# Performance work log

Measured on AMD Instinct MI355X. Metric: run time of the kernel, lower is better.

## Reference

```python
import jax, jax.numpy as jnp
import numpy as np

B, N, DX, DZ, L = 512, 32, 78, 64, 1000

def _gcn_norm(A):
    # PyG gcn_norm: add remaining self loops (fill 1), symmetric D^-1/2 (A+I) D^-1/2
    n = A.shape[-1]
    A_hat = jnp.maximum(A, jnp.eye(n, dtype=A.dtype))
    dinv = jax.lax.rsqrt(A_hat.sum(-1))
    return A_hat * dinv[..., :, None] * dinv[..., None, :]

def _bn(h, g, b, eps=1e-5):
    # BatchNorm1d, training-mode batch statistics (torch default module state)
    m = jnp.mean(h, 0)
    v = jnp.var(h, 0)
    return (h - m) * jax.lax.rsqrt(v + eps) * g + b

def _conv(h, W, b):  # h [B,C,L], W [O,I,K], valid padding + ReLU (Conv1dReLU)
    y = jax.lax.conv_general_dilated(h, W, (1,), 'VALID', dimension_numbers=('NCH', 'OIH', 'NCH'))
    return jax.nn.relu(y + b[None, :, None])

def _attn(v):  # Attention.project is only Tanh in the source
    return jax.nn.softmax(jnp.tanh(v), axis=1) * v

def _forward(x, adj, target, z, dec_W0, dec_b0, dec_g0, dec_be0, dec_W1, dec_b1, dec_g1, dec_be1,
             gW1, gb1, gW2, gb2, gW3, gb3, fcg1_W, fcg1_b, fcg2_W, fcg2_b, emb,
             c10_W, c10_b, c20_W, c20_b, c21_W, c21_b, c30_W, c30_b, c31_W, c31_b, c32_W, c32_b,
             prot_W, prot_b, fc1_W, fc1_b, fc2_W, fc2_b, out_W, out_b):
    Bn = B * N
    # frozen conditional VAE decoder -> augmented features (detached)
    zc = jnp.concatenate([z.reshape(Bn, DZ), x.reshape(Bn, DX)], axis=-1)
    h = jax.nn.relu(_bn(zc @ dec_W0 + dec_b0, dec_g0, dec_be0))
    aug = jnp.tanh(_bn(h @ dec_W1 + dec_b1, dec_g1, dec_be1))
    aug = jax.lax.stop_gradient(aug).reshape(B, N, DX)
    X = jnp.concatenate([aug, x], axis=-1)  # [B,N,156]
    # 1-hop / 2-hop / 3-hop adjacency patterns (spspmm -> binary power patterns)
    A1 = _gcn_norm(adj)
    A2p = (adj @ adj > 0).astype(adj.dtype)
    A3p = (A2p @ adj > 0).astype(adj.dtype)
    A2 = _gcn_norm(A2p)
    A3 = _gcn_norm(A3p)
    gcn = lambda A, hh, W, b: jax.nn.relu(A @ (hh @ W) + b)
    h1 = gcn(A1, X, gW1, gb1)
    h2 = gcn(A1, h1, gW2, gb2)
    h3 = gcn(A1, h2, gW3, gb3)
    h5 = gcn(A2, gcn(A2, X, gW1, gb1), gW2, gb2)
    h6 = gcn(A3, X, gW1, gb1)
    hg = jnp.max(jnp.concatenate([h3, h5, h6], axis=-1), axis=1)  # gmp -> [B,1092]
    xg = jax.nn.relu(hg @ fcg1_W + fcg1_b) @ fcg2_W + fcg2_b  # dropout = identity (eval)
    xg = _attn(xg)
    # protein branch
    e = jnp.transpose(emb[target], (0, 2, 1))  # [B,128,1000]
    f1 = jnp.max(_conv(e, c10_W, c10_b), axis=-1)
    f2 = jnp.max(_conv(_conv(e, c20_W, c20_b), c21_W, c21_b), axis=-1)
    f3 = jnp.max(_conv(_conv(_conv(e, c30_W, c30_b), c31_W, c31_b), c32_W, c32_b), axis=-1)
    xt = _attn(jnp.concatenate([f1, f2, f3], axis=-1) @ prot_W + prot_b)
    xc = jnp.concatenate([xg, xt], axis=-1)
    xc = jax.nn.relu(xc @ fc1_W + fc1_b)
    xc = jax.nn.relu(xc @ fc2_W + fc2_b)
    return xc @ out_W + out_b

def setup_inputs():
    key = jax.random.key(0)
    ks = iter(jax.random.split(key, 64))
    def w(shape, s=0.05):
        return jax.random.normal(next(ks), shape, dtype=jnp.float32) * s
    x = jax.random.normal(next(ks), (B, N, DX), dtype=jnp.float32)
    r = jax.random.uniform(next(ks), (B, N, N))
    up = jnp.triu((r < 0.08).astype(jnp.float32), 1)
    adj = up + jnp.swapaxes(up, 1, 2)  # symmetric, no self loops, avg degree ~5
    target = jax.random.randint(next(ks), (B, L), 0, 26, dtype=jnp.int32)
    z = jax.random.normal(next(ks), (B, N, DZ), dtype=jnp.float32)
    emb = w((26, 128), 1.0).at[0].set(0.0)  # padding_idx=0
    return dict(x=x, adj=adj, target=target, z=z,
        dec_W0=w((DZ + DX, 256)), dec_b0=jnp.zeros(256), dec_g0=jnp.ones(256), dec_be0=jnp.zeros(256),
        dec_W1=w((256, DX)), dec_b1=jnp.zeros(DX), dec_g1=jnp.ones(DX), dec_be1=jnp.zeros(DX),
        gW1=w((156, 156)), gb1=jnp.zeros(156), gW2=w((156, 312)), gb2=jnp.zeros(312),
        gW3=w((312, 624)), gb3=jnp.zeros(624),
        fcg1_W=w((1092, 1024)), fcg1_b=jnp.zeros(1024), fcg2_W=w((1024, 128)), fcg2_b=jnp.zeros(128),
        emb=emb,
        c10_W=w((96, 128, 3)), c10_b=jnp.zeros(96),
        c20_W=w((96, 128, 3)), c20_b=jnp.zeros(96), c21_W=w((96, 96, 3)), c21_b=jnp.zeros(96),
        c30_W=w((96, 128, 3)), c30_b=jnp.zeros(96), c31_W=w((96, 96, 3)), c31_b=jnp.zeros(96),
        c32_W=w((96, 96, 3)), c32_b=jnp.zeros(96),
        prot_W=w((288, 128)), prot_b=jnp.zeros(128),
        fc1_W=w((256, 1024)), fc1_b=jnp.zeros(1024), fc2_W=w((1024, 512)), fc2_b=jnp.zeros(512),
        out_W=w((512, 1)), out_b=jnp.zeros(1))

def reference(x, adj, target, z, dec_W0, dec_b0, dec_g0, dec_be0, dec_W1, dec_b1, dec_g1, dec_be1,
              gW1, gb1, gW2, gb2, gW3, gb3, fcg1_W, fcg1_b, fcg2_W, fcg2_b, emb,
              c10_W, c10_b, c20_W, c20_b, c21_W, c21_b, c30_W, c30_b, c31_W, c31_b, c32_W, c32_b,
              prot_W, prot_b, fc1_W, fc1_b, fc2_W, fc2_b, out_W, out_b):
    return _forward(x, adj, target, z, dec_W0, dec_b0, dec_g0, dec_be0, dec_W1, dec_b1, dec_g1, dec_be1,
                    gW1, gb1, gW2, gb2, gW3, gb3, fcg1_W, fcg1_b, fcg2_W, fcg2_b, emb,
                    c10_W, c10_b, c20_W, c20_b, c21_W, c21_b, c30_W, c30_b, c31_W, c31_b, c32_W, c32_b,
                    prot_W, prot_b, fc1_W, fc1_b, fc2_W, fc2_b, out_W, out_b)
```

## Files before the change

### kernel.cpp

```cpp
#include <hip/hip_runtime.h>

static constexpr size_t O_H0    = 0;
static constexpr size_t O_H1P   = 4194304;
static constexpr size_t O_X     = 5473216;
static constexpr size_t O_A1    = 8029120;
static constexpr size_t O_A2    = 8553408;
static constexpr size_t O_A3    = 9077696;
static constexpr size_t O_H4    = 9601984;
static constexpr size_t O_H6    = 12157888;
static constexpr size_t O_H1W2  = 14713792;
static constexpr size_t O_H2    = 19825600;
static constexpr size_t O_H2W3  = 24937408;
static constexpr size_t O_H3    = 35161024;
static constexpr size_t O_HG    = 45384640;
static constexpr size_t O_FCG1O = 45943744;
static constexpr size_t O_M     = 46468032;
static constexpr size_t O_F     = 46535424;
static constexpr size_t O_V     = 46682880;
static constexpr size_t O_XC    = 46748416;
static constexpr size_t O_FC1O  = 46879488;
static constexpr size_t O_FC2O  = 47403776;
static constexpr size_t O_PART  = 47665920;
static constexpr size_t O_MV    = 47698688;
static constexpr size_t O_BT21  = 47699712;
static constexpr size_t O_BT31  = 47727360;
static constexpr size_t O_W32T  = 47755008;
static constexpr size_t O_XW1  = O_H0;
static constexpr size_t O_SK   = O_H0;
static constexpr size_t O_H1   = O_X;
static constexpr size_t O_H4W2 = O_H1W2;
static constexpr size_t O_H5   = O_H2W3;
static constexpr size_t O_R10  = O_H1W2;
static constexpr size_t O_R20  = O_H1W2 + 1687296;
static constexpr size_t O_R30  = O_H1W2 + 3374592;
static constexpr size_t O_N21  = O_H2W3;
static constexpr size_t O_N31  = O_H2W3 + 5061888;

template<int AMODE, int ACT>
__global__ __launch_bounds__(256) void gemm_k(
    const float* __restrict__ A, const float* __restrict__ Bm,
    const float* __restrict__ bias, float* __restrict__ C,
    int M, int N, int K, const float* __restrict__ A2)
{
  __shared__ __align__(16) float sA[16 * 68];
  __shared__ __align__(16) float sB[16 * 68];
  const int tid = threadIdx.x;
  const int m0 = blockIdx.y * 64, n0 = blockIdx.x * 64;
  const int tx = tid & 15, ty = tid >> 4;
  float acc[4][4] = {};
  for (int k0 = 0; k0 < K; k0 += 16) {
#pragma unroll
    for (int s2 = 0; s2 < 4; s2++) {
      int idx = tid + s2 * 256;
      int am = idx >> 4, ak = idx & 15;
      int gm = m0 + am, gk = k0 + ak;
      float va = 0.f;
      if (gm < M && gk < K) {
        if (AMODE == 0) va = A[(size_t)gm * K + gk];
        else            va = (gk < 64) ? A[gm * 64 + gk] : A2[gm * 78 + gk - 64];
      }
      sA[ak * 68 + am] = va;
      int bk2 = idx >> 6, bn = idx & 63;
      int gk2 = k0 + bk2, gn = n0 + bn;
      float vb = 0.f;
      if (gk2 < K && gn < N) vb = Bm[(size_t)gk2 * N + gn];
      sB[bk2 * 68 + bn] = vb;
    }
    __syncthreads();
#pragma unroll
    for (int kk = 0; kk < 16; kk++) {
      const float4 a4 = *(const float4*)&sA[kk * 68 + ty * 4];
      const float4 b4 = *(const float4*)&sB[kk * 68 + tx * 4];
      const float ra[4] = {a4.x, a4.y, a4.z, a4.w};
      const float rb[4] = {b4.x, b4.y, b4.z, b4.w};
#pragma unroll
      for (int i2 = 0; i2 < 4; i2++)
#pragma unroll
        for (int j2 = 0; j2 < 4; j2++)
          acc[i2][j2] = fmaf(ra[i2], rb[j2], acc[i2][j2]);
    }
    __syncthreads();
  }
#pragma unroll
  for (int i2 = 0; i2 < 4; i2++) {
    int gm = m0 + ty * 4 + i2;
    if (gm >= M) continue;
#pragma unroll
    for (int j2 = 0; j2 < 4; j2++) {
      int gn = n0 + tx * 4 + j2;
      if (gn >= N) continue;
      float v = acc[i2][j2];
      if (bias) v += bias[gn];
      if (ACT == 1) v = fmaxf(v, 0.f);
      C[(size_t)gm * N + gn] = v;
    }
  }
}

__global__ __launch_bounds__(256) void gemm_sk(
    const float* __restrict__ A, const float* __restrict__ Bm,
    float* __restrict__ PT, int M, int N, int K, int KS)
{
  __shared__ __align__(16) float sA[16 * 68];
  __shared__ __align__(16) float sB[16 * 68];
  const int tid = threadIdx.x;
  const int m0 = blockIdx.y * 64, n0 = blockIdx.x * 64;
  const int kb = blockIdx.z * KS;
  const int ke = min(K, kb + KS);
  const int tx = tid & 15, ty = tid >> 4;
  float acc[4][4] = {};
  for (int k0 = kb; k0 < ke; k0 += 16) {
#pragma unroll
    for (int s2 = 0; s2 < 4; s2++) {
      int idx = tid + s2 * 256;
      int am = idx >> 4, ak = idx & 15;
      int gm = m0 + am, gk = k0 + ak;
      float va = 0.f;
      if (gm < M && gk < ke) va = A[(size_t)gm * K + gk];
      sA[ak * 68 + am] = va;
      int bk2 = idx >> 6, bn = idx & 63;
      int gk2 = k0 + bk2, gn = n0 + bn;
      float vb = 0.f;
      if (gk2 < ke && gn < N) vb = Bm[(size_t)gk2 * N + gn];
      sB[bk2 * 68 + bn] = vb;
    }
    __syncthreads();
#pragma unroll
    for (int kk = 0; kk < 16; kk++) {
      const float4 a4 = *(const float4*)&sA[kk * 68 + ty * 4];
      const float4 b4 = *(const float4*)&sB[kk * 68 + tx * 4];
      const float ra[4] = {a4.x, a4.y, a4.z, a4.w};
      const float rb[4] = {b4.x, b4.y, b4.z, b4.w};
#pragma unroll
      for (int i2 = 0; i2 < 4; i2++)
#pragma unroll
        for (int j2 = 0; j2 < 4; j2++)
          acc[i2][j2] = fmaf(ra[i2], rb[j2], acc[i2][j2]);
    }
    __syncthreads();
  }
  float* P = PT + (size_t)blockIdx.z * M * N;
#pragma unroll
  for (int i2 = 0; i2 < 4; i2++) {
    int gm = m0 + ty * 4 + i2;
    if (gm >= M) continue;
#pragma unroll
    for (int j2 = 0; j2 < 4; j2++) {
      int gn = n0 + tx * 4 + j2;
      if (gn >= N) continue;
      P[(size_t)gm * N + gn] = acc[i2][j2];
    }
  }
}

__global__ void skred_kernel(const float* __restrict__ PT, const float* __restrict__ bias,
                             float* __restrict__ C, int MN, int nmask, int S, int act)
{
  int i = blockIdx.x * 256 + threadIdx.x;
  if (i >= MN) return;
  float s = 0.f;
  for (int z = 0; z < S; z++) s += PT[(size_t)z * MN + i];
  if (bias) s += bias[i & nmask];
  if (act) s = fmaxf(s, 0.f);
  C[i] = s;
}

template<int AMODE, int ACT>
__global__ __launch_bounds__(256) void gemm2_k(
    const float* __restrict__ A, const float* __restrict__ Bm,
    const float* __restrict__ bias, float* __restrict__ C,
    int M, int N, int K, const float* __restrict__ A2)
{
  __shared__ __align__(16) float sA[16 * 132];
  __shared__ __align__(16) float sB[16 * 68];
  const int tid = threadIdx.x;
  const int m0 = blockIdx.y * 128, n0 = blockIdx.x * 64;
  const int tx = tid & 15, ty = tid >> 4;
  float acc[8][4] = {};
  for (int k0 = 0; k0 < K; k0 += 16) {
#pragma unroll
    for (int s2 = 0; s2 < 2; s2++) {
      int idx = tid + s2 * 256;
      int am = idx >> 2, kq = idx & 3;
      int gm = m0 + am;
#pragma unroll
      for (int j = 0; j < 4; j++) {
        int gk = k0 + kq * 4 + j;
        float va = 0.f;
        if (gm < M && gk < K) {
          if (AMODE == 0) va = A[(size_t)gm * K + gk];
          else            va = (gk < 64) ? A[gm * 64 + gk] : A2[gm * 78 + gk - 64];
        }
        sA[(kq * 4 + j) * 132 + am] = va;
      }
    }
    {
      int bk = tid >> 4, bn4 = tid & 15;
      int gk2 = k0 + bk;
#pragma unroll
      for (int j = 0; j < 4; j++) {
        int gn = n0 + bn4 * 4 + j;
        float vb = 0.f;
        if (gk2 < K && gn < N) vb = Bm[(size_t)gk2 * N + gn];
        sB[bk * 68 + bn4 * 4 + j] = vb;
      }
    }
    __syncthreads();
#pragma unroll
    for (int kk = 0; kk < 16; kk++) {
      const float4 a0 = *(const float4*)&sA[kk * 132 + ty * 8];
      const float4 a1 = *(const float4*)&sA[kk * 132 + ty * 8 + 4];
      const float4 b4 = *(const float4*)&sB[kk * 68 + tx * 4];
      const float ra[8] = {a0.x, a0.y, a0.z, a0.w, a1.x, a1.y, a1.z, a1.w};
      const float rb[4] = {b4.x, b4.y, b4.z, b4.w};
#pragma unroll
      for (int i2 = 0; i2 < 8; i2++)
#pragma unroll
        for (int j2 = 0; j2 < 4; j2++)
          acc[i2][j2] = fmaf(ra[i2], rb[j2], acc[i2][j2]);
    }
    __syncthreads();
  }
#pragma unroll
  for (int i2 = 0; i2 < 8; i2++) {
    int gm = m0 + ty * 8 + i2;
    if (gm >= M) continue;
#pragma unroll
    for (int j2 = 0; j2 < 4; j2++) {
      int gn = n0 + tx * 4 + j2;
      if (gn >= N) continue;
      float v = acc[i2][j2];
      if (bias) v += bias[gn];
      if (ACT == 1) v = fmaxf(v, 0.f);
      C[(size_t)gm * N + gn] = v;
    }
  }
}

template<int AMODE, int ACT>
__global__ __launch_bounds__(256) void gemm3_k(
    const float* __restrict__ A, const float* __restrict__ Bm,
    const float* __restrict__ bias, float* __restrict__ C,
    int M, int N, int K, const float* __restrict__ A2)
{
  __shared__ __align__(16) float sA[16][132];
  __shared__ __align__(16) float sB[16][132];
  const int tid = threadIdx.x;
  const int m0 = blockIdx.y * 128, n0 = blockIdx.x * 128;
  const int tx = tid & 15, ty = tid >> 4;
  float acc[8][8] = {};
  for (int k0 = 0; k0 < K; k0 += 16) {
    {
      int am = tid >> 1;
      int kq = (tid & 1) * 8;
      int gm = m0 + am;
#pragma unroll
      for (int j = 0; j < 8; j++) {
        int gk = k0 + kq + j;
        float va = 0.f;
        if (gm < M && gk < K) {
          if (AMODE == 0) va = A[(size_t)gm * K + gk];
          else            va = (gk < 64) ? A[gm * 64 + gk] : A2[gm * 78 + gk - 64];
        }
        sA[kq + j][am] = va;
      }
      int bk = tid >> 4;
      int bn = (tid & 15) * 8;
      int gk2 = k0 + bk;
#pragma unroll
      for (int j = 0; j < 8; j++) {
        int gn = n0 + bn + j;
        float vb = 0.f;
        if (gk2 < K && gn < N) vb = Bm[(size_t)gk2 * N + gn];
        sB[bk][bn + j] = vb;
      }
    }
    __syncthreads();
#pragma unroll
    for (int kk = 0; kk < 16; kk++) {
      const float4 a0 = *(const float4*)&sA[kk][ty * 4];
      const float4 a1 = *(const float4*)&sA[kk][64 + ty * 4];
      const float4 b0 = *(const float4*)&sB[kk][tx * 4];
      const float4 b1 = *(const float4*)&sB[kk][64 + tx * 4];
      const float ra[8] = {a0.x, a0.y, a0.z, a0.w, a1.x, a1.y, a1.z, a1.w};
      const float rb[8] = {b0.x, b0.y, b0.z, b0.w, b1.x, b1.y, b1.z, b1.w};
#pragma unroll
      for (int i = 0; i < 8; i++)
#pragma unroll
        for (int j = 0; j < 8; j++)
          acc[i][j] = fmaf(ra[i], rb[j], acc[i][j]);
    }
    __syncthreads();
  }
#pragma unroll
  for (int i = 0; i < 8; i++) {
    int gm = m0 + (i < 4 ? ty * 4 + i : 64 + ty * 4 + (i - 4));
    if (gm >= M) continue;
#pragma unroll
    for (int j = 0; j < 8; j++) {
      int gn = n0 + (j < 4 ? tx * 4 + j : 64 + tx * 4 + (j - 4));
      if (gn >= N) continue;
      float v = acc[i][j];
      if (bias) v += bias[gn];
      if (ACT == 1) v = fmaxf(v, 0.f);
      C[(size_t)gm * N + gn] = v;
    }
  }
}

__global__ __launch_bounds__(256) void bn_partial(const float* __restrict__ H,
    float* __restrict__ PS, float* __restrict__ PQ, int C)
{
  int c = blockIdx.x * 64 + (threadIdx.x & 63);
  int rg = threadIdx.x >> 6;
  __shared__ float sS[256], sQ[256];
  float s = 0.f, q = 0.f;
  if (c < C) {
    int base = blockIdx.y * 256 + rg;
    for (int t = 0; t < 64; t++) {
      float v = H[(size_t)(base + 4 * t) * C + c];
      s += v; q += v * v;
    }
  }
  sS[threadIdx.x] = s; sQ[threadIdx.x] = q;
  __syncthreads();
  if (threadIdx.x < 64 && c < C) {
    float ts = sS[threadIdx.x] + sS[threadIdx.x + 64] + sS[threadIdx.x + 128] + sS[threadIdx.x + 192];
    float tq = sQ[threadIdx.x] + sQ[threadIdx.x + 64] + sQ[threadIdx.x + 128] + sQ[threadIdx.x + 192];
    PS[blockIdx.y * C + c] = ts;
    PQ[blockIdx.y * C + c] = tq;
  }
}

__global__ void bn_final(const float* __restrict__ PS, const float* __restrict__ PQ,
                         float* __restrict__ MV, int C)
{
  int c = threadIdx.x;
  if (c >= C) return;
  float s = 0.f, q = 0.f;
  for (int y = 0; y < 64; y++) { s += PS[y * C + c]; q += PQ[y * C + c]; }
  float mean = s * (1.f / 16384.f);
  float var = q * (1.f / 16384.f) - mean * mean;
  MV[c] = mean; MV[256 + c] = var;
}

__global__ void bn_norm(const float* __restrict__ IN, float* __restrict__ OUT,
                        const float* __restrict__ MV, const float* __restrict__ g,
                        const float* __restrict__ bb, int C, int ostride, int total, int act)
{
  int idx = blockIdx.x * 256 + threadIdx.x;
  if (idx >= total) return;
  int r = idx / C, c = idx - r * C;
  float v = (IN[idx] - MV[c]) * (1.f / sqrtf(MV[256 + c] + 1e-5f)) * g[c] + bb[c];
  v = (act == 1) ? fmaxf(v, 0.f) : tanhf(v);
  OUT[(size_t)r * ostride + c] = v;
}

__global__ void xcopy_kernel(const float* __restrict__ x, float* __restrict__ X)
{
  int idx = blockIdx.x * 256 + threadIdx.x;
  if (idx >= 16384 * 78) return;
  int r = idx / 78, j = idx - r * 78;
  X[(size_t)r * 156 + 78 + j] = x[idx];
}

__global__ __launch_bounds__(1024) void adj_kernel(const float* __restrict__ adj,
    float* __restrict__ A1o, float* __restrict__ A2o, float* __restrict__ A3o)
{
  int b = blockIdx.x, t = threadIdx.x;
  int i = t >> 5, j = t & 31;
  __shared__ float sA[32][33], sP[32][33];
  __shared__ float sd1[32], sd2[32], sd3[32];
  float a = adj[b * 1024 + t];
  sA[i][j] = a;
  float ah = (i == j) ? fmaxf(a, 1.f) : a;
  float rs = ah;
#pragma unroll
  for (int m = 16; m >= 1; m >>= 1) rs += __shfl_xor(rs, m, 32);
  float di = 1.f / sqrtf(rs);
  if (j == 0) sd1[i] = di;
  __syncthreads();
  A1o[b * 1024 + t] = ah * di * sd1[j];
  float c2 = 0.f;
#pragma unroll
  for (int k = 0; k < 32; k++) c2 += sA[i][k] * sA[k][j];
  float p2 = (c2 > 0.f) ? 1.f : 0.f;
  sP[i][j] = p2;
  float ah2 = (i == j) ? 1.f : p2;
  float rs2 = ah2;
#pragma unroll
  for (int m = 16; m >= 1; m >>= 1) rs2 += __shfl_xor(rs2, m, 32);
  float di2 = 1.f / sqrtf(rs2);
  if (j == 0) sd2[i] = di2;
  __syncthreads();
  A2o[b * 1024 + t] = ah2 * di2 * sd2[j];
  float c3 = 0.f;
#pragma unroll
  for (int k = 0; k < 32; k++) c3 += sP[i][k] * sA[k][j];
  float p3 = (c3 > 0.f) ? 1.f : 0.f;
  float ah3 = (i == j) ? 1.f : p3;
  float rs3 = ah3;
#pragma unroll
  for (int m = 16; m >= 1; m >>= 1) rs3 += __shfl_xor(rs3, m, 32);
  float di3 = 1.f / sqrtf(rs3);
  if (j == 0) sd3[i] = di3;
  __syncthreads();
  A3o[b * 1024 + t] = ah3 * di3 * sd3[j];
}

__global__ __launch_bounds__(64) void agg_kernel(const float* __restrict__ A,
    const float* __restrict__ HW, const float* __restrict__ bias,
    float* __restrict__ OUT, int C)
{
  int b = blockIdx.y;
  int c = blockIdx.x * 64 + threadIdx.x;
  __shared__ float sAd[1024];
  for (int e = threadIdx.x; e < 1024; e += 64) sAd[e] = A[b * 1024 + e];
  __syncthreads();
  if (c >= C) return;
  float hw[32];
  const float* hp = HW + (size_t)b * 32 * C + c;
#pragma unroll
  for (int m = 0; m < 32; m++) hw[m] = hp[(size_t)m * C];
  float bv = bias[c];
#pragma unroll 2
  for (int n = 0; n < 32; n++) {
    float s = bv;
#pragma unroll
    for (int m = 0; m < 32; m++) s = fmaf(sAd[n * 32 + m], hw[m], s);
    OUT[(size_t)b * 32 * C + (size_t)n * C + c] = fmaxf(s, 0.f);
  }
}

__global__ void hg_kernel(const float* __restrict__ h3, const float* __restrict__ h5,
                          const float* __restrict__ h6, float* __restrict__ HG)
{
  int b = blockIdx.y;
  int c = blockIdx.x * 256 + threadIdx.x;
  if (c >= 1092) return;
  const float* p; int stride;
  if (c < 624)      { p = h3 + (size_t)b * 32 * 624 + c;          stride = 624; }
  else if (c < 936) { p = h5 + (size_t)b * 32 * 312 + (c - 624);  stride = 312; }
  else              { p = h6 + (size_t)b * 32 * 156 + (c - 936);  stride = 156; }
  float m = p[0];
#pragma unroll 4
  for (int n = 1; n < 32; n++) m = fmaxf(m, p[(size_t)n * stride]);
  HG[b * 1092 + c] = m;
}

__global__ __launch_bounds__(64) void attn_kernel(const float* __restrict__ V,
    float* __restrict__ OUT, int ostride, int ooff)
{
  int r = blockIdx.x, lane = threadIdx.x;
  float v0 = V[r * 128 + lane], v1 = V[r * 128 + 64 + lane];
  float e0 = expf(tanhf(v0)), e1 = expf(tanhf(v1));
  float s = e0 + e1;
#pragma unroll
  for (int m = 32; m >= 1; m >>= 1) s += __shfl_xor(s, m);
  float inv = 1.f / s;
  OUT[r * ostride + ooff + lane] = e0 * inv * v0;
  OUT[r * ostride + ooff + 64 + lane] = e1 * inv * v1;
}

__global__ void mtable_kernel(const float* __restrict__ emb, const float* __restrict__ W10,
    const float* __restrict__ W20, const float* __restrict__ W30, float* __restrict__ M)
{
  int idx = blockIdx.x * 256 + threadIdx.x;
  if (idx >= 3 * 3 * 26 * 96) return;
  int o = idx % 96, tok = (idx / 96) % 26, k = (idx / (96 * 26)) % 3, cv = idx / (96 * 26 * 3);
  const float* W = (cv == 0) ? W10 : ((cv == 1) ? W20 : W30);
  float s = 0.f;
#pragma unroll 4
  for (int i = 0; i < 128; i++) s = fmaf(emb[tok * 128 + i], W[(o * 128 + i) * 3 + k], s);
  M[idx] = s;
}

__global__ void rtable_kernel(const float* __restrict__ M,
    const float* __restrict__ b1, const float* __restrict__ b2, const float* __restrict__ b3,
    float* __restrict__ R1, float* __restrict__ R2, float* __restrict__ R3)
{
  int cv = blockIdx.y;
  int idx = blockIdx.x * 256 + threadIdx.x;
  if (idx >= 17576 * 96) return;
  int o = idx % 96, g = idx / 96;
  int t0 = g / 676, t1 = (g / 26) % 26, t2 = g % 26;
  const float* Mc = M + cv * 3 * 26 * 96;
  float v = ((cv == 0) ? b1 : ((cv == 1) ? b2 : b3))[o];
  v += Mc[(0 * 26 + t0) * 96 + o] + Mc[(1 * 26 + t1) * 96 + o] + Mc[(2 * 26 + t2) * 96 + o];
  float* R = (cv == 0) ? R1 : ((cv == 1) ? R2 : R3);
  R[idx] = fmaxf(v, 0.f);
}

__global__ void wtrans_kernel(const float* __restrict__ W, float* __restrict__ out, int mode)
{
  int e = blockIdx.x * 256 + threadIdx.x;
  if (e >= 96 * 96 * 3) return;
  int o, i, k;
  if (mode == 0) { i = e / 288; int r = e % 288; k = r / 96; o = r % 96; }
  else           { k = e / (96 * 96); i = (e / 96) % 96; o = e % 96; }
  out[e] = W[(o * 96 + i) * 3 + k];
}

__global__ __launch_bounds__(384) void conv3_fused(const int* __restrict__ target,
    const float* __restrict__ R10,
    const float* __restrict__ N21, const float* __restrict__ b21,
    const float* __restrict__ N31, const float* __restrict__ b31,
    const float* __restrict__ W32t, const float* __restrict__ b32, float* __restrict__ F)
{
  int b = blockIdx.y, tile = blockIdx.x;
  int l0 = tile * 64;
  int tid = threadIdx.x;
  __shared__ float sIn[96 * 67];
  __shared__ int sG[68];
  __shared__ float sR1[4 * 96], sR2[4 * 96];
  int ncols = min(66, 996 - l0);
  int n1    = min(66, 998 - l0);
  int nouts = min(64, 994 - l0);
  int ng    = min(68, 998 - l0);
  for (int p = tid; p < ng; p += 384) {
    int t0 = target[b * 1000 + l0 + p];
    int t1 = target[b * 1000 + l0 + p + 1];
    int t2 = target[b * 1000 + l0 + p + 2];
    sG[p] = (t0 * 26 + t1) * 26 + t2;
  }
  __syncthreads();
  {
    int i = tid % 96;
    int coff = tid / 96;
    float v1m = 0.f, v2m = 0.f;
    for (int c = coff; c < n1; c += 4) {
      v1m = fmaxf(v1m, R10[(size_t)sG[c] * 96 + i]);
      if (c < ncols) {
        int g0 = sG[c], g1 = sG[c + 1], g2 = sG[c + 2];
        float n3 = b31[i]
                 + N31[((size_t)g0 * 3 + 0) * 96 + i]
                 + N31[((size_t)g1 * 3 + 1) * 96 + i]
                 + N31[((size_t)g2 * 3 + 2) * 96 + i];
        sIn[i * 67 + c] = fmaxf(n3, 0.f);
        float n2 = b21[i]
                 + N21[((size_t)g0 * 3 + 0) * 96 + i]
                 + N21[((size_t)g1 * 3 + 1) * 96 + i]
                 + N21[((size_t)g2 * 3 + 2) * 96 + i];
        v2m = fmaxf(v2m, fmaxf(n2, 0.f));
      }
    }
    sR1[coff * 96 + i] = v1m;
    sR2[coff * 96 + i] = v2m;
  }
  __syncthreads();
  if (tid < 192) {
    int which = tid / 96, i = tid % 96;
    const float* r = which ? sR2 : sR1;
    float m = fmaxf(fmaxf(r[i], r[96 + i]), fmaxf(r[192 + i], r[288 + i]));
    atomicMax((unsigned int*)&F[b * 288 + which * 96 + i], __float_as_uint(m));
  }
  int wv = __builtin_amdgcn_readfirstlane(tid >> 6);
  int lane = tid & 63;
  int obase = wv * 16;
  float acc[16];
#pragma unroll
  for (int jj = 0; jj < 16; jj++) acc[jj] = b32[obase + jj];
#pragma unroll 1
  for (int k = 0; k < 3; k++) {
#pragma unroll 4
    for (int i = 0; i < 96; i++) {
      float xv = sIn[i * 67 + lane + k];
      const float* wp = W32t + ((size_t)(k * 96 + i)) * 96 + obase;
#pragma unroll
      for (int jj = 0; jj < 16; jj++) acc[jj] = fmaf(xv, wp[jj], acc[jj]);
    }
  }
  bool lok = lane < nouts;
#pragma unroll
  for (int jj = 0; jj < 16; jj++) {
    float v = lok ? fmaxf(acc[jj], 0.f) : 0.f;
#pragma unroll
    for (int m = 32; m >= 1; m >>= 1) v = fmaxf(v, __shfl_xor(v, m));
    if (lane == 0) atomicMax((unsigned int*)&F[b * 288 + 192 + obase + jj], __float_as_uint(v));
  }
}

__global__ __launch_bounds__(256) void outdot_kernel(const float* __restrict__ X,
    const float* __restrict__ W, const float* __restrict__ bptr, float* __restrict__ out)
{
  int r = blockIdx.x * 4 + (threadIdx.x >> 6);
  int lane = threadIdx.x & 63;
  float s = 0.f;
  for (int j = lane; j < 512; j += 64) s = fmaf(X[(size_t)r * 512 + j], W[j], s);
#pragma unroll
  for (int m = 32; m >= 1; m >>= 1) s += __shfl_xor(s, m);
  if (lane == 0) out[r] = s + bptr[0];
}

static inline void gemm(hipStream_t st, int AMODE, int ACT,
                        const float* A, const float* B, const float* bias, float* C,
                        int M, int N, int K, const float* A2 = nullptr)
{
  dim3 g((N + 63) / 64, (M + 63) / 64), blk(256);
  if (AMODE == 0 && ACT == 0)      gemm_k<0, 0><<<g, blk, 0, st>>>(A, B, bias, C, M, N, K, A2);
  else if (AMODE == 0 && ACT == 1) gemm_k<0, 1><<<g, blk, 0, st>>>(A, B, bias, C, M, N, K, A2);
  else                             gemm_k<1, 0><<<g, blk, 0, st>>>(A, B, bias, C, M, N, K, A2);
}

static inline void gemm2(hipStream_t st, int AMODE, int ACT,
                         const float* A, const float* B, const float* bias, float* C,
                         int M, int N, int K, const float* A2 = nullptr)
{
  dim3 g((N + 63) / 64, (M + 127) / 128), blk(256);
  if (AMODE == 0 && ACT == 0)      gemm2_k<0, 0><<<g, blk, 0, st>>>(A, B, bias, C, M, N, K, A2);
  else if (AMODE == 0 && ACT == 1) gemm2_k<0, 1><<<g, blk, 0, st>>>(A, B, bias, C, M, N, K, A2);
  else                             gemm2_k<1, 0><<<g, blk, 0, st>>>(A, B, bias, C, M, N, K, A2);
}

static inline void gemm3(hipStream_t st, int AMODE, int ACT,
                         const float* A, const float* B, const float* bias, float* C,
                         int M, int N, int K, const float* A2 = nullptr)
{
  dim3 g((N + 127) / 128, (M + 127) / 128), blk(256);
  if (AMODE == 0 && ACT == 0)      gemm3_k<0, 0><<<g, blk, 0, st>>>(A, B, bias, C, M, N, K, A2);
  else if (AMODE == 0 && ACT == 1) gemm3_k<0, 1><<<g, blk, 0, st>>>(A, B, bias, C, M, N, K, A2);
  else                             gemm3_k<1, 0><<<g, blk, 0, st>>>(A, B, bias, C, M, N, K, A2);
}

static inline void gemm_splitk(hipStream_t st, const float* A, const float* B,
                               const float* bias, float* C, int M, int N, int K,
                               int S, int act, float* PT)
{
  int KS = (K + S - 1) / S;
  dim3 g((N + 63) / 64, (M + 63) / 64, S);
  gemm_sk<<<g, 256, 0, st>>>(A, B, PT, M, N, K, KS);
  int MN = M * N;
  skred_kernel<<<(MN + 255) / 256, 256, 0, st>>>(PT, bias, C, MN, N - 1, S, act);
}

extern "C" void kernel_launch(void* const* d_in, const int* in_sizes, int n_in,
                              void* d_out, int out_size, void* d_ws, size_t ws_size,
                              hipStream_t stream)
{
  (void)in_sizes; (void)n_in; (void)out_size; (void)ws_size;
  const float* x      = (const float*)d_in[0];
  const float* adj    = (const float*)d_in[1];
  const int*   target = (const int*)  d_in[2];
  const float* z      = (const float*)d_in[3];
  const float* dec_W0 = (const float*)d_in[4];
  const float* dec_b0 = (const float*)d_in[5];
  const float* dec_g0 = (const float*)d_in[6];
  const float* dec_be0= (const float*)d_in[7];
  const float* dec_W1 = (const float*)d_in[8];
  const float* dec_b1 = (const float*)d_in[9];
  const float* dec_g1 = (const float*)d_in[10];
  const float* dec_be1= (const float*)d_in[11];
  const float* gW1    = (const float*)d_in[12];
  const float* gb1    = (const float*)d_in[13];
  const float* gW2    = (const float*)d_in[14];
  const float* gb2    = (const float*)d_in[15];
  const float* gW3    = (const float*)d_in[16];
  const float* gb3    = (const float*)d_in[17];
  const float* fcg1_W = (const float*)d_in[18];
  const float* fcg1_b = (const float*)d_in[19];
  const float* fcg2_W = (const float*)d_in[20];
  const float* fcg2_b = (const float*)d_in[21];
  const float* emb    = (const float*)d_in[22];
  const float* c10_W  = (const float*)d_in[23];
  const float* c10_b  = (const float*)d_in[24];
  const float* c20_W  = (const float*)d_in[25];
  const float* c20_b  = (const float*)d_in[26];
  const float* c21_W  = (const float*)d_in[27];
  const float* c21_b  = (const float*)d_in[28];
  const float* c30_W  = (const float*)d_in[29];
  const float* c30_b  = (const float*)d_in[30];
  const float* c31_W  = (const float*)d_in[31];
  const float* c31_b  = (const float*)d_in[32];
  const float* c32_W  = (const float*)d_in[33];
  const float* c32_b  = (const float*)d_in[34];
  const float* prot_W = (const float*)d_in[35];
  const float* prot_b = (const float*)d_in[36];
  const float* fc1_W  = (const float*)d_in[37];
  const float* fc1_b  = (const float*)d_in[38];
  const float* fc2_W  = (const float*)d_in[39];
  const float* fc2_b  = (const float*)d_in[40];
  const float* out_W  = (const float*)d_in[41];
  const float* out_b  = (const float*)d_in[42];
  float* out = (float*)d_out;
  float* ws = (float*)d_ws;

  float* H0   = ws + O_H0;   float* H1P  = ws + O_H1P;  float* X    = ws + O_X;
  float* A1   = ws + O_A1;   float* A2   = ws + O_A2;   float* A3   = ws + O_A3;
  float* XW1  = ws + O_XW1;  float* H1   = ws + O_H1;   float* H4   = ws + O_H4;
  float* H6   = ws + O_H6;   float* H1W2 = ws + O_H1W2; float* H2   = ws + O_H2;
  float* H2W3 = ws + O_H2W3; float* H3   = ws + O_H3;   float* H4W2 = ws + O_H4W2;
  float* H5   = ws + O_H5;   float* HG   = ws + O_HG;   float* FCG1O= ws + O_FCG1O;
  float* Mt   = ws + O_M;    float* F    = ws + O_F;    float* V    = ws + O_V;
  float* XC   = ws + O_XC;   float* FC1O = ws + O_FC1O; float* FC2O = ws + O_FC2O;
  float* PS   = ws + O_PART; float* PQ   = ws + O_PART + 16384;
  float* MV   = ws + O_MV;   float* SK   = ws + O_SK;
  float* R10  = ws + O_R10;  float* R20  = ws + O_R20;  float* R30  = ws + O_R30;
  float* N21  = ws + O_N21;  float* N31  = ws + O_N31;
  float* BT21 = ws + O_BT21; float* BT31 = ws + O_BT31; float* W32T = ws + O_W32T;

  gemm3(stream, 1, 0, z, dec_W0, dec_b0, H0, 16384, 256, 142, x);
  bn_partial<<<dim3(4, 64), 256, 0, stream>>>(H0, PS, PQ, 256);
  bn_final<<<1, 256, 0, stream>>>(PS, PQ, MV, 256);
  bn_norm<<<16384, 256, 0, stream>>>(H0, H0, MV, dec_g0, dec_be0, 256, 256, 16384 * 256, 1);
  gemm2(stream, 0, 0, H0, dec_W1, dec_b1, H1P, 16384, 78, 256);
  bn_partial<<<dim3(2, 64), 256, 0, stream>>>(H1P, PS, PQ, 78);
  bn_final<<<1, 256, 0, stream>>>(PS, PQ, MV, 78);
  bn_norm<<<4995, 256, 0, stream>>>(H1P, X, MV, dec_g1, dec_be1, 78, 156, 16384 * 78, 2);
  xcopy_kernel<<<4995, 256, 0, stream>>>(x, X);

  adj_kernel<<<512, 1024, 0, stream>>>(adj, A1, A2, A3);

  gemm2(stream, 0, 0, X, gW1, nullptr, XW1, 16384, 156, 156);
  agg_kernel<<<dim3(3, 512), 64, 0, stream>>>(A1, XW1, gb1, H1, 156);
  agg_kernel<<<dim3(3, 512), 64, 0, stream>>>(A2, XW1, gb1, H4, 156);
  agg_kernel<<<dim3(3, 512), 64, 0, stream>>>(A3, XW1, gb1, H6, 156);
  gemm2(stream, 0, 0, H1, gW2, nullptr, H1W2, 16384, 312, 156);
  agg_kernel<<<dim3(5, 512), 64, 0, stream>>>(A1, H1W2, gb2, H2, 312);
  gemm3(stream, 0, 0, H2, gW3, nullptr, H2W3, 16384, 624, 312);
  agg_kernel<<<dim3(10, 512), 64, 0, stream>>>(A1, H2W3, gb3, H3, 624);
  gemm2(stream, 0, 0, H4, gW2, nullptr, H4W2, 16384, 312, 156);
  agg_kernel<<<dim3(5, 512), 64, 0, stream>>>(A2, H4W2, gb2, H5, 312);
  hg_kernel<<<dim3(5, 512), 256, 0, stream>>>(H3, H5, H6, HG);

  gemm_splitk(stream, HG, fcg1_W, fcg1_b, FCG1O, 512, 1024, 1092, 4, 1, SK);
  gemm_splitk(stream, FCG1O, fcg2_W, fcg2_b, V, 512, 128, 1024, 8, 0, SK);
  attn_kernel<<<512, 64, 0, stream>>>(V, XC, 256, 0);

  hipMemsetAsync(F, 0, 512 * 288 * sizeof(float), stream);
  mtable_kernel<<<264, 256, 0, stream>>>(emb, c10_W, c20_W, c30_W, Mt);
  rtable_kernel<<<dim3(6591, 3), 256, 0, stream>>>(Mt, c10_b, c20_b, c30_b, R10, R20, R30);
  wtrans_kernel<<<108, 256, 0, stream>>>(c21_W, BT21, 0);
  wtrans_kernel<<<108, 256, 0, stream>>>(c31_W, BT31, 0);
  wtrans_kernel<<<108, 256, 0, stream>>>(c32_W, W32T, 1);
  gemm2(stream, 0, 0, R20, BT21, nullptr, N21, 17576, 288, 96);
  gemm2(stream, 0, 0, R30, BT31, nullptr, N31, 17576, 288, 96);
  conv3_fused<<<dim3(16, 512), 384, 0, stream>>>(target, R10, N21, c21_b, N31, c31_b, W32T, c32_b, F);
  gemm_splitk(stream, F, prot_W, prot_b, V, 512, 128, 288, 4, 0, SK);
  attn_kernel<<<512, 64, 0, stream>>>(V, XC, 256, 128);

  gemm_splitk(stream, XC, fc1_W, fc1_b, FC1O, 512, 1024, 256, 2, 1, SK);
  gemm_splitk(stream, FC1O, fc2_W, fc2_b, FC2O, 512, 512, 1024, 4, 1, SK);
  outdot_kernel<<<128, 256, 0, stream>>>(FC2O, out_W, out_b, out);
}
```

Measured before the change: 1.412 ms.

## Fuse x-copy into batchnorm, merge weight transposes, vectorize conv gathers, retune GEMM variants

```diff
diff --git a/kernel.cpp b/kernel.cpp
--- a/kernel.cpp
+++ b/kernel.cpp
@@ -346,7 +346,8 @@
 
 __global__ void bn_norm(const float* __restrict__ IN, float* __restrict__ OUT,
                         const float* __restrict__ MV, const float* __restrict__ g,
-                        const float* __restrict__ bb, int C, int ostride, int total, int act)
+                        const float* __restrict__ bb, int C, int ostride, int total, int act,
+                        const float* __restrict__ xsrc)
 {
   int idx = blockIdx.x * 256 + threadIdx.x;
   if (idx >= total) return;
@@ -354,14 +355,7 @@
   float v = (IN[idx] - MV[c]) * (1.f / sqrtf(MV[256 + c] + 1e-5f)) * g[c] + bb[c];
   v = (act == 1) ? fmaxf(v, 0.f) : tanhf(v);
   OUT[(size_t)r * ostride + c] = v;
-}
-
-__global__ void xcopy_kernel(const float* __restrict__ x, float* __restrict__ X)
-{
-  int idx = blockIdx.x * 256 + threadIdx.x;
-  if (idx >= 16384 * 78) return;
-  int r = idx / 78, j = idx - r * 78;
-  X[(size_t)r * 156 + 78 + j] = x[idx];
+  if (xsrc) OUT[(size_t)r * ostride + 78 + c] = xsrc[idx];
 }
 
 __global__ __launch_bounds__(1024) void adj_kernel(const float* __restrict__ adj,
@@ -491,13 +485,19 @@
   R[idx] = fmaxf(v, 0.f);
 }
 
-__global__ void wtrans_kernel(const float* __restrict__ W, float* __restrict__ out, int mode)
+__global__ void wtrans3_kernel(const float* __restrict__ W21, const float* __restrict__ W31,
+                               const float* __restrict__ W32,
+                               float* __restrict__ O21, float* __restrict__ O31,
+                               float* __restrict__ O32)
 {
   int e = blockIdx.x * 256 + threadIdx.x;
   if (e >= 96 * 96 * 3) return;
+  int job = blockIdx.y;
+  const float* W = (job == 0) ? W21 : ((job == 1) ? W31 : W32);
+  float* out = (job == 0) ? O21 : ((job == 1) ? O31 : O32);
   int o, i, k;
-  if (mode == 0) { i = e / 288; int r = e % 288; k = r / 96; o = r % 96; }
-  else           { k = e / (96 * 96); i = (e / 96) % 96; o = e % 96; }
+  if (job < 2) { i = e / 288; int r = e % 288; k = r / 96; o = r % 96; }
+  else         { k = e / (96 * 96); i = (e / 96) % 96; o = e % 96; }
   out[e] = W[(o * 96 + i) * 3 + k];
 }
 
@@ -512,11 +512,12 @@
   int tid = threadIdx.x;
   __shared__ float sIn[96 * 67];
   __shared__ int sG[68];
-  __shared__ float sR1[4 * 96], sR2[4 * 96];
+  __shared__ unsigned sR[192];
   int ncols = min(66, 996 - l0);
   int n1    = min(66, 998 - l0);
   int nouts = min(64, 994 - l0);
   int ng    = min(68, 998 - l0);
+  if (tid < 192) sR[tid] = 0u;
   for (int p = tid; p < ng; p += 384) {
     int t0 = target[b * 1000 + l0 + p];
     int t1 = target[b * 1000 + l0 + p + 1];
@@ -525,34 +526,50 @@
   }
   __syncthreads();
   {
-    int i = tid % 96;
-    int coff = tid / 96;
-    float v1m = 0.f, v2m = 0.f;
-    for (int c = coff; c < n1; c += 4) {
-      v1m = fmaxf(v1m, R10[(size_t)sG[c] * 96 + i]);
+    int ig = tid % 24;
+    int coff = tid / 24;
+    int i4 = ig * 4;
+    float4 v1m = make_float4(0.f, 0.f, 0.f, 0.f);
+    float4 v2m = make_float4(0.f, 0.f, 0.f, 0.f);
+    const float4 bb31 = *(const float4*)&b31[i4];
+    const float4 bb21 = *(const float4*)&b21[i4];
+    for (int c = coff; c < n1; c += 16) {
+      float4 r1 = *(const float4*)&R10[(size_t)sG[c] * 96 + i4];
+      v1m.x = fmaxf(v1m.x, r1.x); v1m.y = fmaxf(v1m.y, r1.y);
+      v1m.z = fmaxf(v1m.z, r1.z); v1m.w = fmaxf(v1m.w, r1.w);
       if (c < ncols) {
-        int g0 = sG[c], g1 = sG[c + 1], g2 = sG[c + 2];
-        float n3 = b31[i]
-                 + N31[((size_t)g0 * 3 + 0) * 96 + i]
-                 + N31[((size_t)g1 * 3 + 1) * 96 + i]
-                 + N31[((size_t)g2 * 3 + 2) * 96 + i];
-        sIn[i * 67 + c] = fmaxf(n3, 0.f);
-        float n2 = b21[i]
-                 + N21[((size_t)g0 * 3 + 0) * 96 + i]
-                 + N21[((size_t)g1 * 3 + 1) * 96 + i]
-                 + N21[((size_t)g2 * 3 + 2) * 96 + i];
-        v2m = fmaxf(v2m, fmaxf(n2, 0.f));
+        size_t r0 = (size_t)sG[c] * 3 + 0;
+        size_t r1i = (size_t)sG[c + 1] * 3 + 1;
+        size_t r2 = (size_t)sG[c + 2] * 3 + 2;
+        float4 a0 = *(const float4*)&N31[r0 * 96 + i4];
+        float4 a1 = *(const float4*)&N31[r1i * 96 + i4];
+        float4 a2 = *(const float4*)&N31[r2 * 96 + i4];
+        sIn[(i4 + 0) * 67 + c] = fmaxf(bb31.x + a0.x + a1.x + a2.x, 0.f);
+        sIn[(i4 + 1) * 67 + c] = fmaxf(bb31.y + a0.y + a1.y + a2.y, 0.f);
+        sIn[(i4 + 2) * 67 + c] = fmaxf(bb31.z + a0.z + a1.z + a2.z, 0.f);
+        sIn[(i4 + 3) * 67 + c] = fmaxf(bb31.w + a0.w + a1.w + a2.w, 0.f);
+        float4 c0 = *(const float4*)&N21[r0 * 96 + i4];
+        float4 c1 = *(const float4*)&N21[r1i * 96 + i4];
+        float4 c2 = *(const float4*)&N21[r2 * 96 + i4];
+        v2m.x = fmaxf(v2m.x, bb21.x + c0.x + c1.x + c2.x);
+        v2m.y = fmaxf(v2m.y, bb21.y + c0.y + c1.y + c2.y);
+        v2m.z = fmaxf(v2m.z, bb21.z + c0.z + c1.z + c2.z);
+        v2m.w = fmaxf(v2m.w, bb21.w + c0.w + c1.w + c2.w);
       }
     }
-    sR1[coff * 96 + i] = v1m;
-    sR2[coff * 96 + i] = v2m;
+    atomicMax(&sR[i4 + 0], __float_as_uint(v1m.x));
+    atomicMax(&sR[i4 + 1], __float_as_uint(v1m.y));
+    atomicMax(&sR[i4 + 2], __float_as_uint(v1m.z));
+    atomicMax(&sR[i4 + 3], __float_as_uint(v1m.w));
+    atomicMax(&sR[96 + i4 + 0], __float_as_uint(fmaxf(v2m.x, 0.f)));
+    atomicMax(&sR[96 + i4 + 1], __float_as_uint(fmaxf(v2m.y, 0.f)));
+    atomicMax(&sR[96 + i4 + 2], __float_as_uint(fmaxf(v2m.z, 0.f)));
+    atomicMax(&sR[96 + i4 + 3], __float_as_uint(fmaxf(v2m.w, 0.f)));
   }
   __syncthreads();
   if (tid < 192) {
     int which = tid / 96, i = tid % 96;
-    const float* r = which ? sR2 : sR1;
-    float m = fmaxf(fmaxf(r[i], r[96 + i]), fmaxf(r[192 + i], r[288 + i]));
-    atomicMax((unsigned int*)&F[b * 288 + which * 96 + i], __float_as_uint(m));
+    atomicMax((unsigned int*)&F[b * 288 + which * 96 + i], sR[tid]);
   }
   int wv = __builtin_amdgcn_readfirstlane(tid >> 6);
   int lane = tid & 63;
@@ -698,15 +715,14 @@
   float* N21  = ws + O_N21;  float* N31  = ws + O_N31;
   float* BT21 = ws + O_BT21; float* BT31 = ws + O_BT31; float* W32T = ws + O_W32T;
 
-  gemm3(stream, 1, 0, z, dec_W0, dec_b0, H0, 16384, 256, 142, x);
+  gemm2(stream, 1, 0, z, dec_W0, dec_b0, H0, 16384, 256, 142, x);
   bn_partial<<<dim3(4, 64), 256, 0, stream>>>(H0, PS, PQ, 256);
   bn_final<<<1, 256, 0, stream>>>(PS, PQ, MV, 256);
-  bn_norm<<<16384, 256, 0, stream>>>(H0, H0, MV, dec_g0, dec_be0, 256, 256, 16384 * 256, 1);
+  bn_norm<<<16384, 256, 0, stream>>>(H0, H0, MV, dec_g0, dec_be0, 256, 256, 16384 * 256, 1, nullptr);
   gemm2(stream, 0, 0, H0, dec_W1, dec_b1, H1P, 16384, 78, 256);
   bn_partial<<<dim3(2, 64), 256, 0, stream>>>(H1P, PS, PQ, 78);
   bn_final<<<1, 256, 0, stream>>>(PS, PQ, MV, 78);
-  bn_norm<<<4995, 256, 0, stream>>>(H1P, X, MV, dec_g1, dec_be1, 78, 156, 16384 * 78, 2);
-  xcopy_kernel<<<4995, 256, 0, stream>>>(x, X);
+  bn_norm<<<4995, 256, 0, stream>>>(H1P, X, MV, dec_g1, dec_be1, 78, 156, 16384 * 78, 2, x);
 
   adj_kernel<<<512, 1024, 0, stream>>>(adj, A1, A2, A3);
 
@@ -714,11 +730,11 @@
   agg_kernel<<<dim3(3, 512), 64, 0, stream>>>(A1, XW1, gb1, H1, 156);
   agg_kernel<<<dim3(3, 512), 64, 0, stream>>>(A2, XW1, gb1, H4, 156);
   agg_kernel<<<dim3(3, 512), 64, 0, stream>>>(A3, XW1, gb1, H6, 156);
-  gemm2(stream, 0, 0, H1, gW2, nullptr, H1W2, 16384, 312, 156);
+  gemm3(stream, 0, 0, H1, gW2, nullptr, H1W2, 16384, 312, 156);
   agg_kernel<<<dim3(5, 512), 64, 0, stream>>>(A1, H1W2, gb2, H2, 312);
   gemm3(stream, 0, 0, H2, gW3, nullptr, H2W3, 16384, 624, 312);
   agg_kernel<<<dim3(10, 512), 64, 0, stream>>>(A1, H2W3, gb3, H3, 624);
-  gemm2(stream, 0, 0, H4, gW2, nullptr, H4W2, 16384, 312, 156);
+  gemm3(stream, 0, 0, H4, gW2, nullptr, H4W2, 16384, 312, 156);
   agg_kernel<<<dim3(5, 512), 64, 0, stream>>>(A2, H4W2, gb2, H5, 312);
   hg_kernel<<<dim3(5, 512), 256, 0, stream>>>(H3, H5, H6, HG);
 
@@ -729,11 +745,9 @@
   hipMemsetAsync(F, 0, 512 * 288 * sizeof(float), stream);
   mtable_kernel<<<264, 256, 0, stream>>>(emb, c10_W, c20_W, c30_W, Mt);
   rtable_kernel<<<dim3(6591, 3), 256, 0, stream>>>(Mt, c10_b, c20_b, c30_b, R10, R20, R30);
-  wtrans_kernel<<<108, 256, 0, stream>>>(c21_W, BT21, 0);
-  wtrans_kernel<<<108, 256, 0, stream>>>(c31_W, BT31, 0);
-  wtrans_kernel<<<108, 256, 0, stream>>>(c32_W, W32T, 1);
-  gemm2(stream, 0, 0, R20, BT21, nullptr, N21, 17576, 288, 96);
-  gemm2(stream, 0, 0, R30, BT31, nullptr, N31, 17576, 288, 96);
+  wtrans3_kernel<<<dim3(108, 3), 256, 0, stream>>>(c21_W, c31_W, c32_W, BT21, BT31, W32T);
+  gemm3(stream, 0, 0, R20, BT21, nullptr, N21, 17576, 288, 96);
+  gemm3(stream, 0, 0, R30, BT31, nullptr, N31, 17576, 288, 96);
   conv3_fused<<<dim3(16, 512), 384, 0, stream>>>(target, R10, N21, c21_b, N31, c31_b, W32T, c32_b, F);
   gemm_splitk(stream, F, prot_W, prot_b, V, 512, 128, 288, 4, 0, SK);
   attn_kernel<<<512, 64, 0, stream>>>(V, XC, 256, 128);
```

Result: faster. 1.376 ms (-2.6%).
